# Kernel tuning notes

Hardware: AMD Instinct MI355X
Metric: run time of the kernel (lower is better)

Reference implementation:

```python
import jax, jax.numpy as jnp
import numpy as np

H = 256  # rnn_size


def setup_inputs() -> dict:
    key = jax.random.key(0)
    ks = jax.random.split(key, 6)
    B, T, F, D = 64, 512, 64, 64
    s_in = 1.0 / np.sqrt(F)
    s_rec = 1.0 / np.sqrt(H)
    return {
        "x": jax.random.normal(ks[0], (B, T, F), jnp.float32),
        "kernel": jax.random.normal(ks[1], (F, 3 * H), jnp.float32) * s_in,
        "recurrent_kernel": jax.random.normal(ks[2], (H, 3 * H), jnp.float32) * s_rec,
        "bias": jax.random.normal(ks[3], (3 * H,), jnp.float32) * 0.01,
        "dense_w": jax.random.normal(ks[4], (H, D), jnp.float32) * s_rec,
        "dense_b": jax.random.normal(ks[5], (D,), jnp.float32) * 0.01,
    }


def _gru_scan(x, kernel, recurrent_kernel, bias):
    B, T, _ = x.shape
    # Pre-project all timesteps: [B, T, 3H]
    xproj = jnp.einsum("btf,fg->btg", x, kernel) + bias
    xproj_t = jnp.transpose(xproj, (1, 0, 2))  # [T, B, 3H]

    def step(h, xt):
        # Keras GRU, reset_after=False: r gates the recurrent matmul of the candidate
        rec = h @ recurrent_kernel  # [B, 3H]
        xz, xr, xh = xt[:, :H], xt[:, H:2 * H], xt[:, 2 * H:]
        rz, rr, rh = rec[:, :H], rec[:, H:2 * H], rec[:, 2 * H:]
        z = jax.nn.sigmoid(xz + rz)
        r = jax.nn.sigmoid(xr + rr)
        hh = jnp.tanh(xh + r * rh)
        h_new = z * h + (1.0 - z) * hh
        return h_new, h_new

    h0 = jnp.zeros((B, H), x.dtype)
    h_last, outs = jax.lax.scan(step, h0, xproj_t)
    return jnp.transpose(outs, (1, 0, 2)), h_last  # [B,T,H], [B,H]


def reference(x, kernel, recurrent_kernel, bias, dense_w, dense_b):
    outputs, h_last = _gru_scan(x, kernel, recurrent_kernel, bias)
    state = jnp.tanh(h_last @ dense_w + dense_b)  # [B, dense_size]
    return outputs, state
```

## Files before the change

### kernel.cpp

```cpp
#include <hip/hip_runtime.h>


typedef _Float16 half2_t __attribute__((ext_vector_type(2)));
typedef _Float16 f16x4_t __attribute__((ext_vector_type(4)));

#define LOG2E 1.4426950408889634f

__device__ __forceinline__ float fast_sigmoid(float x) {
  float e = __builtin_amdgcn_exp2f(-x * LOG2E);
  return __builtin_amdgcn_rcpf(1.0f + e);
}
__device__ __forceinline__ float fast_tanh(float x) {
  float e = __builtin_amdgcn_exp2f(x * (2.0f * LOG2E));
  return 1.0f - 2.0f * __builtin_amdgcn_rcpf(1.0f + e);
}

__global__ __launch_bounds__(256, 4) void xproj_gemm(
    const float* __restrict__ x, const float* __restrict__ kmat,
    const float* __restrict__ bias, _Float16* __restrict__ xp) {
  __shared__ half2_t As2[32][132];
  __shared__ half2_t Bs2[32][132];
  const int tid = threadIdx.x;
  const int rb = blockIdx.x * 128;
  const int cb = blockIdx.y * 128;

  {
    const int k4 = (tid & 15) * 4;
    const int r0 = tid >> 4;
#pragma unroll
    for (int p = 0; p < 8; ++p) {
      int r = r0 + p * 16;
      float4 v = *(const float4*)(x + (size_t)(rb + r) * 64 + k4);
      half2_t lo, hi;
      lo[0] = (_Float16)v.x; lo[1] = (_Float16)v.y;
      hi[0] = (_Float16)v.z; hi[1] = (_Float16)v.w;
      As2[k4 / 2][r] = lo;
      As2[k4 / 2 + 1][r] = hi;
    }
  }
  {
    const int c4 = (tid & 31) * 4;
    const int kp0 = tid >> 5;
#pragma unroll
    for (int p = 0; p < 4; ++p) {
      int kp = kp0 + p * 8;
      float4 va = *(const float4*)(kmat + (size_t)(2 * kp) * 768 + cb + c4);
      float4 vb = *(const float4*)(kmat + (size_t)(2 * kp + 1) * 768 + cb + c4);
      half2_t o0, o1, o2, o3;
      o0[0] = (_Float16)va.x; o0[1] = (_Float16)vb.x;
      o1[0] = (_Float16)va.y; o1[1] = (_Float16)vb.y;
      o2[0] = (_Float16)va.z; o2[1] = (_Float16)vb.z;
      o3[0] = (_Float16)va.w; o3[1] = (_Float16)vb.w;
      Bs2[kp][c4 + 0] = o0;
      Bs2[kp][c4 + 1] = o1;
      Bs2[kp][c4 + 2] = o2;
      Bs2[kp][c4 + 3] = o3;
    }
  }
  __syncthreads();

  const int tx = tid & 15, ty = tid >> 4;
  const int r0 = ty * 8;
  const int c0 = tx * 4;
  float acc[8][8];
  {
    float4 b0 = *(const float4*)(bias + cb + c0);
    float4 b1 = *(const float4*)(bias + cb + 64 + c0);
    float bz[8] = {b0.x, b0.y, b0.z, b0.w, b1.x, b1.y, b1.z, b1.w};
#pragma unroll
    for (int i = 0; i < 8; ++i)
#pragma unroll
      for (int j = 0; j < 8; ++j) acc[i][j] = bz[j];
  }

#pragma unroll 2
  for (int kp = 0; kp < 32; ++kp) {
    half2_t a2[8], b2[8];
    *(int4*)(&a2[0]) = *(const int4*)(&As2[kp][r0]);
    *(int4*)(&a2[4]) = *(const int4*)(&As2[kp][r0 + 4]);
    *(int2*)(&b2[0]) = *(const int2*)(&Bs2[kp][c0]);
    *(int2*)(&b2[2]) = *(const int2*)(&Bs2[kp][c0 + 2]);
    *(int2*)(&b2[4]) = *(const int2*)(&Bs2[kp][64 + c0]);
    *(int2*)(&b2[6]) = *(const int2*)(&Bs2[kp][64 + c0 + 2]);
#pragma unroll
    for (int i = 0; i < 8; ++i)
#pragma unroll
      for (int j = 0; j < 8; ++j)
        acc[i][j] = __builtin_amdgcn_fdot2(a2[i], b2[j], acc[i][j], false);
  }

#pragma unroll
  for (int i = 0; i < 8; ++i) {
    f16x4_t o0, o1;
#pragma unroll
    for (int j = 0; j < 4; ++j) {
      o0[j] = (_Float16)acc[i][j];
      o1[j] = (_Float16)acc[i][4 + j];
    }
    _Float16* dst = xp + (size_t)(rb + r0 + i) * 768 + cb;
    *(f16x4_t*)(dst + c0) = o0;
    *(f16x4_t*)(dst + 64 + c0) = o1;
  }
}

__global__ __launch_bounds__(1024, 4) void gru_scan(
    const _Float16* __restrict__ xp, const float* __restrict__ wr,
    const float* __restrict__ dw, const float* __restrict__ db,
    float* __restrict__ out, float* __restrict__ state) {
  __shared__ float part[4 * 768];
  __shared__ float hbuf[256];
  __shared__ alignas(16) _Float16 hhalf[256];
  __shared__ _Float16 xrow[768];

  const int tid = threadIdx.x;
  const int b = blockIdx.x;
  const int c = tid >> 8;
  const int col = tid & 255;

  half2_t w2[3][32];
#pragma unroll
  for (int q = 0; q < 3; ++q) {
    const float* wp = wr + (size_t)(c * 64) * 768 + col + q * 256;
#pragma unroll
    for (int j = 0; j < 32; ++j) {
      float wa = wp[(size_t)(2 * j) * 768];
      float wb = wp[(size_t)(2 * j + 1) * 768];
      half2_t p;
      p[0] = (_Float16)wa;
      p[1] = (_Float16)wb;
      w2[q][j] = p;
    }
  }

  if (tid < 256) hhalf[tid] = (_Float16)0.0f;
  __syncthreads();

  const _Float16* xpb = xp + (size_t)b * 512 * 768;
  float* outb = out + (size_t)b * 512 * 256;
  const int4* hp2 = (const int4*)hhalf + c * 8;
  float hprev = 0.0f;

  for (int t = 0; t < 512; ++t) {
    _Float16 xv = (_Float16)0.0f;
    if (tid < 768) xv = xpb[(size_t)t * 768 + tid];

    float a0 = 0.0f, a1 = 0.0f, a2 = 0.0f;
    int4 hv = hp2[0];
#pragma unroll
    for (int g = 0; g < 8; ++g) {
      __builtin_amdgcn_sched_barrier(1);
      int4 hn = hv;
      if (g < 7) hn = hp2[g + 1];
      half2_t p0 = __builtin_bit_cast(half2_t, hv.x);
      half2_t p1 = __builtin_bit_cast(half2_t, hv.y);
      half2_t p2 = __builtin_bit_cast(half2_t, hv.z);
      half2_t p3 = __builtin_bit_cast(half2_t, hv.w);
      a0 = __builtin_amdgcn_fdot2(p0, w2[0][g * 4 + 0], a0, false);
      a0 = __builtin_amdgcn_fdot2(p1, w2[0][g * 4 + 1], a0, false);
      a0 = __builtin_amdgcn_fdot2(p2, w2[0][g * 4 + 2], a0, false);
      a0 = __builtin_amdgcn_fdot2(p3, w2[0][g * 4 + 3], a0, false);
      a1 = __builtin_amdgcn_fdot2(p0, w2[1][g * 4 + 0], a1, false);
      a1 = __builtin_amdgcn_fdot2(p1, w2[1][g * 4 + 1], a1, false);
      a1 = __builtin_amdgcn_fdot2(p2, w2[1][g * 4 + 2], a1, false);
      a1 = __builtin_amdgcn_fdot2(p3, w2[1][g * 4 + 3], a1, false);
      a2 = __builtin_amdgcn_fdot2(p0, w2[2][g * 4 + 0], a2, false);
      a2 = __builtin_amdgcn_fdot2(p1, w2[2][g * 4 + 1], a2, false);
      a2 = __builtin_amdgcn_fdot2(p2, w2[2][g * 4 + 2], a2, false);
      a2 = __builtin_amdgcn_fdot2(p3, w2[2][g * 4 + 3], a2, false);
      hv = hn;
    }
    part[c * 768 + col] = a0;
    part[c * 768 + col + 256] = a1;
    part[c * 768 + col + 512] = a2;
    if (tid < 768) xrow[tid] = xv;
    __syncthreads();

    if (tid < 256) {
      const int i = tid;
      if (t) outb[(size_t)(t - 1) * 256 + i] = hprev;
      float rz = part[i] + part[768 + i] + part[1536 + i] + part[2304 + i];
      float rr = part[256 + i] + part[768 + 256 + i] + part[1536 + 256 + i] +
                 part[2304 + 256 + i];
      float rh = part[512 + i] + part[768 + 512 + i] + part[1536 + 512 + i] +
                 part[2304 + 512 + i];
      float xz = (float)xrow[i];
      float xr = (float)xrow[256 + i];
      float xh = (float)xrow[512 + i];
      float z = fast_sigmoid(xz + rz);
      float r = fast_sigmoid(xr + rr);
      float hh = fast_tanh(xh + r * rh);
      float hnew = z * hprev + (1.0f - z) * hh;
      hprev = hnew;
      hhalf[i] = (_Float16)hnew;
    }
    __syncthreads();
  }

  if (tid < 256) {
    outb[(size_t)511 * 256 + tid] = hprev;
    hbuf[tid] = hprev;
  }
  __syncthreads();

  if (tid < 64) {
    float acc = db[tid];
#pragma unroll 8
    for (int k = 0; k < 256; ++k) acc = fmaf(hbuf[k], dw[k * 64 + tid], acc);
    state[(size_t)b * 64 + tid] = fast_tanh(acc);
  }
}

extern "C" void kernel_launch(void* const* d_in, const int* in_sizes, int n_in,
                              void* d_out, int out_size, void* d_ws,
                              size_t ws_size, hipStream_t stream) {
  const float* x = (const float*)d_in[0];
  const float* kmat = (const float*)d_in[1];
  const float* wr = (const float*)d_in[2];
  const float* bias = (const float*)d_in[3];
  const float* dw = (const float*)d_in[4];
  const float* db = (const float*)d_in[5];

  float* out = (float*)d_out;
  float* state = out + (size_t)64 * 512 * 256;
  _Float16* xp = (_Float16*)d_ws;

  dim3 gg(32768 / 128, 768 / 128);
  xproj_gemm<<<gg, 256, 0, stream>>>(x, kmat, bias, xp);
  gru_scan<<<64, 1024, 0, stream>>>(xp, wr, dw, db, out, state);
}
```

Measured before the change: 662.3 us.

## Reduce GRU recurrent partials with DPP in registers and double-buffer hidden state

Reorganizes the scan kernel so each lane covers a 32-element K-slice for six gate columns. The K-split partial sums are now reduced across lanes with DPP shuffles instead of through a shared-memory partial buffer. The hidden state is double-buffered in padded shared memory, which cuts each timestep from two barriers to one and drops the xrow staging. The trade-offs are more per-lane accumulators and select logic, and only a quarter of the lanes doing the gate math.

Result: slower. 964.9 us (+45.7%).

```diff
diff --git a/kernel.cpp b/kernel.cpp
--- a/kernel.cpp
+++ b/kernel.cpp
@@ -13,6 +13,13 @@
 __device__ __forceinline__ float fast_tanh(float x) {
   float e = __builtin_amdgcn_exp2f(x * (2.0f * LOG2E));
   return 1.0f - 2.0f * __builtin_amdgcn_rcpf(1.0f + e);
+}
+
+template <int CTRL>
+__device__ __forceinline__ float dpp_xor_add(float v) {
+  int s = __builtin_amdgcn_update_dpp(0, __builtin_bit_cast(int, v), CTRL,
+                                      0xF, 0xF, false);
+  return v + __builtin_bit_cast(float, s);
 }
 
 __global__ __launch_bounds__(256, 4) void xproj_gemm(
@@ -103,102 +110,143 @@
   }
 }
 
+#define DOT4(U, J)                                                \
+  do {                                                            \
+    half2_t p0 = __builtin_bit_cast(half2_t, (U).x);              \
+    half2_t p1 = __builtin_bit_cast(half2_t, (U).y);              \
+    half2_t p2 = __builtin_bit_cast(half2_t, (U).z);              \
+    half2_t p3 = __builtin_bit_cast(half2_t, (U).w);               \
+    a0 = __builtin_amdgcn_fdot2(p0, w2[0][(J) + 0], a0, false);   \
+    a0 = __builtin_amdgcn_fdot2(p1, w2[0][(J) + 1], a0, false);   \
+    a0 = __builtin_amdgcn_fdot2(p2, w2[0][(J) + 2], a0, false);   \
+    a0 = __builtin_amdgcn_fdot2(p3, w2[0][(J) + 3], a0, false);   \
+    a1 = __builtin_amdgcn_fdot2(p0, w2[1][(J) + 0], a1, false);   \
+    a1 = __builtin_amdgcn_fdot2(p1, w2[1][(J) + 1], a1, false);   \
+    a1 = __builtin_amdgcn_fdot2(p2, w2[1][(J) + 2], a1, false);   \
+    a1 = __builtin_amdgcn_fdot2(p3, w2[1][(J) + 3], a1, false);   \
+    a2 = __builtin_amdgcn_fdot2(p0, w2[2][(J) + 0], a2, false);   \
+    a2 = __builtin_amdgcn_fdot2(p1, w2[2][(J) + 1], a2, false);   \
+    a2 = __builtin_amdgcn_fdot2(p2, w2[2][(J) + 2], a2, false);   \
+    a2 = __builtin_amdgcn_fdot2(p3, w2[2][(J) + 3], a2, false);   \
+    a3 = __builtin_amdgcn_fdot2(p0, w2[3][(J) + 0], a3, false);   \
+    a3 = __builtin_amdgcn_fdot2(p1, w2[3][(J) + 1], a3, false);   \
+    a3 = __builtin_amdgcn_fdot2(p2, w2[3][(J) + 2], a3, false);   \
+    a3 = __builtin_amdgcn_fdot2(p3, w2[3][(J) + 3], a3, false);   \
+    a4 = __builtin_amdgcn_fdot2(p0, w2[4][(J) + 0], a4, false);   \
+    a4 = __builtin_amdgcn_fdot2(p1, w2[4][(J) + 1], a4, false);   \
+    a4 = __builtin_amdgcn_fdot2(p2, w2[4][(J) + 2], a4, false);   \
+    a4 = __builtin_amdgcn_fdot2(p3, w2[4][(J) + 3], a4, false);   \
+    a5 = __builtin_amdgcn_fdot2(p0, w2[5][(J) + 0], a5, false);   \
+    a5 = __builtin_amdgcn_fdot2(p1, w2[5][(J) + 1], a5, false);   \
+    a5 = __builtin_amdgcn_fdot2(p2, w2[5][(J) + 2], a5, false);   \
+    a5 = __builtin_amdgcn_fdot2(p3, w2[5][(J) + 3], a5, false);   \
+  } while (0)
+
 __global__ __launch_bounds__(1024, 4) void gru_scan(
     const _Float16* __restrict__ xp, const float* __restrict__ wr,
     const float* __restrict__ dw, const float* __restrict__ db,
     float* __restrict__ out, float* __restrict__ state) {
-  __shared__ float part[4 * 768];
+  __shared__ alignas(16) _Float16 hh[2][8][40];
   __shared__ float hbuf[256];
-  __shared__ alignas(16) _Float16 hhalf[256];
-  __shared__ _Float16 xrow[768];
 
   const int tid = threadIdx.x;
   const int b = blockIdx.x;
-  const int c = tid >> 8;
-  const int col = tid & 255;
-
-  half2_t w2[3][32];
-#pragma unroll
-  for (int q = 0; q < 3; ++q) {
-    const float* wp = wr + (size_t)(c * 64) * 768 + col + q * 256;
-#pragma unroll
-    for (int j = 0; j < 32; ++j) {
-      float wa = wp[(size_t)(2 * j) * 768];
-      float wb = wp[(size_t)(2 * j + 1) * 768];
+  const int lane = tid & 63;
+  const int wave = tid >> 6;
+  const int c = (lane & 3) | ((lane >> 1) & 4);
+  const int sidx = ((lane >> 2) & 1) | ((lane >> 3) & 6);
+  const int cidx = wave * 8 + sidx;
+  const int hb = (lane >> 3) & 1;
+  const bool gl = ((lane & 3) == 0);
+  const int col = cidx + hb * 128;
+
+  half2_t w2[6][16];
+#pragma unroll
+  for (int q = 0; q < 6; ++q) {
+    const int g = q % 3, hbq = q / 3;
+    const float* wp = wr + (size_t)(c * 32) * 768 + g * 256 + cidx + hbq * 128;
+#pragma unroll
+    for (int j = 0; j < 16; ++j) {
       half2_t p;
-      p[0] = (_Float16)wa;
-      p[1] = (_Float16)wb;
+      p[0] = (_Float16)wp[(size_t)(2 * j) * 768];
+      p[1] = (_Float16)wp[(size_t)(2 * j + 1) * 768];
       w2[q][j] = p;
     }
   }
 
-  if (tid < 256) hhalf[tid] = (_Float16)0.0f;
+  if (tid < 640) ((_Float16*)hh)[tid] = (_Float16)0.0f;
   __syncthreads();
 
-  const _Float16* xpb = xp + (size_t)b * 512 * 768;
-  float* outb = out + (size_t)b * 512 * 256;
-  const int4* hp2 = (const int4*)hhalf + c * 8;
+  const _Float16* xp_b = xp + (size_t)b * 512 * 768;
+  float* out_b = out + (size_t)b * 512 * 256;
+
   float hprev = 0.0f;
-
+  int buf = 0;
+
+#pragma unroll 1
   for (int t = 0; t < 512; ++t) {
-    _Float16 xv = (_Float16)0.0f;
-    if (tid < 768) xv = xpb[(size_t)t * 768 + tid];
-
-    float a0 = 0.0f, a1 = 0.0f, a2 = 0.0f;
-    int4 hv = hp2[0];
-#pragma unroll
-    for (int g = 0; g < 8; ++g) {
-      __builtin_amdgcn_sched_barrier(1);
-      int4 hn = hv;
-      if (g < 7) hn = hp2[g + 1];
-      half2_t p0 = __builtin_bit_cast(half2_t, hv.x);
-      half2_t p1 = __builtin_bit_cast(half2_t, hv.y);
-      half2_t p2 = __builtin_bit_cast(half2_t, hv.z);
-      half2_t p3 = __builtin_bit_cast(half2_t, hv.w);
-      a0 = __builtin_amdgcn_fdot2(p0, w2[0][g * 4 + 0], a0, false);
-      a0 = __builtin_amdgcn_fdot2(p1, w2[0][g * 4 + 1], a0, false);
-      a0 = __builtin_amdgcn_fdot2(p2, w2[0][g * 4 + 2], a0, false);
-      a0 = __builtin_amdgcn_fdot2(p3, w2[0][g * 4 + 3], a0, false);
-      a1 = __builtin_amdgcn_fdot2(p0, w2[1][g * 4 + 0], a1, false);
-      a1 = __builtin_amdgcn_fdot2(p1, w2[1][g * 4 + 1], a1, false);
-      a1 = __builtin_amdgcn_fdot2(p2, w2[1][g * 4 + 2], a1, false);
-      a1 = __builtin_amdgcn_fdot2(p3, w2[1][g * 4 + 3], a1, false);
-      a2 = __builtin_amdgcn_fdot2(p0, w2[2][g * 4 + 0], a2, false);
-      a2 = __builtin_amdgcn_fdot2(p1, w2[2][g * 4 + 1], a2, false);
-      a2 = __builtin_amdgcn_fdot2(p2, w2[2][g * 4 + 2], a2, false);
-      a2 = __builtin_amdgcn_fdot2(p3, w2[2][g * 4 + 3], a2, false);
-      hv = hn;
-    }
-    part[c * 768 + col] = a0;
-    part[c * 768 + col + 256] = a1;
-    part[c * 768 + col + 512] = a2;
-    if (tid < 768) xrow[tid] = xv;
+    _Float16 x0h = (_Float16)0.0f, x1h = (_Float16)0.0f, x2h = (_Float16)0.0f;
+    if (gl) {
+      if (t) out_b[(size_t)(t - 1) * 256 + col] = hprev;
+      const _Float16* xr_ = xp_b + (size_t)t * 768 + col;
+      x0h = xr_[0];
+      x1h = xr_[256];
+      x2h = xr_[512];
+    }
+
+    const int4* hp = (const int4*)hh[buf][c];
+    float a0 = 0.f, a1 = 0.f, a2 = 0.f, a3 = 0.f, a4 = 0.f, a5 = 0.f;
+    {
+      int4 u0 = hp[0];
+      int4 u1 = hp[1];
+      DOT4(u0, 0);
+      DOT4(u1, 4);
+    }
+    __builtin_amdgcn_sched_barrier(0);
+    {
+      int4 u2 = hp[2];
+      int4 u3 = hp[3];
+      DOT4(u2, 8);
+      DOT4(u3, 12);
+    }
+
+    a0 = dpp_xor_add<0xB1>(a0);
+    a1 = dpp_xor_add<0xB1>(a1);
+    a2 = dpp_xor_add<0xB1>(a2);
+    a3 = dpp_xor_add<0xB1>(a3);
+    a4 = dpp_xor_add<0xB1>(a4);
+    a5 = dpp_xor_add<0xB1>(a5);
+    a0 = dpp_xor_add<0x4E>(a0);
+    a1 = dpp_xor_add<0x4E>(a1);
+    a2 = dpp_xor_add<0x4E>(a2);
+    a3 = dpp_xor_add<0x4E>(a3);
+    a4 = dpp_xor_add<0x4E>(a4);
+    a5 = dpp_xor_add<0x4E>(a5);
+    a0 = dpp_xor_add<0x128>(a0);
+    a1 = dpp_xor_add<0x128>(a1);
+    a2 = dpp_xor_add<0x128>(a2);
+    a3 = dpp_xor_add<0x128>(a3);
+    a4 = dpp_xor_add<0x128>(a4);
+    a5 = dpp_xor_add<0x128>(a5);
+
+    if (gl) {
+      float rz = hb ? a3 : a0;
+      float rr = hb ? a4 : a1;
+      float rh = hb ? a5 : a2;
+      float z = fast_sigmoid((float)x0h + rz);
+      float r = fast_sigmoid((float)x1h + rr);
+      float hcand = fast_tanh((float)x2h + r * rh);
+      float hnew = z * hprev + (1.0f - z) * hcand;
+      hprev = hnew;
+      hh[buf ^ 1][col >> 5][col & 31] = (_Float16)hnew;
+    }
     __syncthreads();
-
-    if (tid < 256) {
-      const int i = tid;
-      if (t) outb[(size_t)(t - 1) * 256 + i] = hprev;
-      float rz = part[i] + part[768 + i] + part[1536 + i] + part[2304 + i];
-      float rr = part[256 + i] + part[768 + 256 + i] + part[1536 + 256 + i] +
-                 part[2304 + 256 + i];
-      float rh = part[512 + i] + part[768 + 512 + i] + part[1536 + 512 + i] +
-                 part[2304 + 512 + i];
-      float xz = (float)xrow[i];
-      float xr = (float)xrow[256 + i];
-      float xh = (float)xrow[512 + i];
-      float z = fast_sigmoid(xz + rz);
-      float r = fast_sigmoid(xr + rr);
-      float hh = fast_tanh(xh + r * rh);
-      float hnew = z * hprev + (1.0f - z) * hh;
-      hprev = hnew;
-      hhalf[i] = (_Float16)hnew;
-    }
-    __syncthreads();
-  }
-
-  if (tid < 256) {
-    outb[(size_t)511 * 256 + tid] = hprev;
-    hbuf[tid] = hprev;
+    buf ^= 1;
+  }
+
+  if (gl) {
+    out_b[(size_t)511 * 256 + col] = hprev;
+    hbuf[col] = hprev;
   }
   __syncthreads();
 
```

## Compute GRU recurrent matvec with MFMA and double-buffered hidden state

Applied to the files above, without the earlier changes.

The recurrent h@W step now runs on 16x16x32 f16 MFMA instructions. Each of 16 waves owns 16 output columns and keeps its weight slice in registers. The A operand's only nonzero row holds h, so most of each MFMA's work is padding. Double-buffering the hidden state removes one of the two block barriers per timestep, and the cross-wave partial-sum reduction through shared memory goes away. In exchange, only 16 lanes per wave run the gate math and load x, and most of the MFMA throughput is spent on zeros.

Result: slower. 733.9 us (+10.8%).

```diff
diff --git a/kernel.cpp b/kernel.cpp
--- a/kernel.cpp
+++ b/kernel.cpp
@@ -3,6 +3,8 @@
 
 typedef _Float16 half2_t __attribute__((ext_vector_type(2)));
 typedef _Float16 f16x4_t __attribute__((ext_vector_type(4)));
+typedef _Float16 f16x8_t __attribute__((ext_vector_type(8)));
+typedef float f32x4_t __attribute__((ext_vector_type(4)));
 
 #define LOG2E 1.4426950408889634f
 
@@ -107,98 +109,84 @@
     const _Float16* __restrict__ xp, const float* __restrict__ wr,
     const float* __restrict__ dw, const float* __restrict__ db,
     float* __restrict__ out, float* __restrict__ state) {
-  __shared__ float part[4 * 768];
+  __shared__ alignas(16) _Float16 zz[256];
+  __shared__ alignas(16) _Float16 hh0[256];
+  __shared__ alignas(16) _Float16 hh1[256];
   __shared__ float hbuf[256];
-  __shared__ alignas(16) _Float16 hhalf[256];
-  __shared__ _Float16 xrow[768];
 
   const int tid = threadIdx.x;
   const int b = blockIdx.x;
-  const int c = tid >> 8;
-  const int col = tid & 255;
-
-  half2_t w2[3][32];
-#pragma unroll
-  for (int q = 0; q < 3; ++q) {
-    const float* wp = wr + (size_t)(c * 64) * 768 + col + q * 256;
-#pragma unroll
-    for (int j = 0; j < 32; ++j) {
-      float wa = wp[(size_t)(2 * j) * 768];
-      float wb = wp[(size_t)(2 * j + 1) * 768];
-      half2_t p;
-      p[0] = (_Float16)wa;
-      p[1] = (_Float16)wb;
-      w2[q][j] = p;
-    }
-  }
-
-  if (tid < 256) hhalf[tid] = (_Float16)0.0f;
+  const int lane = tid & 63;
+  const int w = tid >> 6;
+  const int q = lane >> 4;
+  const int col = w * 16 + (lane & 15);
+  const bool gl = (lane < 16);
+
+  f16x8_t wf[3][8];
+#pragma unroll
+  for (int g = 0; g < 3; ++g)
+#pragma unroll
+    for (int s = 0; s < 8; ++s) {
+      const float* wp = wr + (size_t)(s * 32 + q * 8) * 768 + g * 256 + col;
+      f16x8_t v;
+#pragma unroll
+      for (int j = 0; j < 8; ++j) v[j] = (_Float16)wp[(size_t)j * 768];
+      wf[g][s] = v;
+    }
+
+  if (tid < 256) {
+    zz[tid] = (_Float16)0.0f;
+    hh0[tid] = (_Float16)0.0f;
+  }
   __syncthreads();
+
+  const bool arow0 = ((lane & 15) == 0);
+  const _Float16* ab0 = (arow0 ? hh0 : zz) + q * 8;
+  const _Float16* ab1 = (arow0 ? hh1 : zz) + q * 8;
 
   const _Float16* xpb = xp + (size_t)b * 512 * 768;
   float* outb = out + (size_t)b * 512 * 256;
-  const int4* hp2 = (const int4*)hhalf + c * 8;
   float hprev = 0.0f;
 
+#pragma unroll 2
   for (int t = 0; t < 512; ++t) {
-    _Float16 xv = (_Float16)0.0f;
-    if (tid < 768) xv = xpb[(size_t)t * 768 + tid];
-
-    float a0 = 0.0f, a1 = 0.0f, a2 = 0.0f;
-    int4 hv = hp2[0];
-#pragma unroll
-    for (int g = 0; g < 8; ++g) {
-      __builtin_amdgcn_sched_barrier(1);
-      int4 hn = hv;
-      if (g < 7) hn = hp2[g + 1];
-      half2_t p0 = __builtin_bit_cast(half2_t, hv.x);
-      half2_t p1 = __builtin_bit_cast(half2_t, hv.y);
-      half2_t p2 = __builtin_bit_cast(half2_t, hv.z);
-      half2_t p3 = __builtin_bit_cast(half2_t, hv.w);
-      a0 = __builtin_amdgcn_fdot2(p0, w2[0][g * 4 + 0], a0, false);
-      a0 = __builtin_amdgcn_fdot2(p1, w2[0][g * 4 + 1], a0, false);
-      a0 = __builtin_amdgcn_fdot2(p2, w2[0][g * 4 + 2], a0, false);
-      a0 = __builtin_amdgcn_fdot2(p3, w2[0][g * 4 + 3], a0, false);
-      a1 = __builtin_amdgcn_fdot2(p0, w2[1][g * 4 + 0], a1, false);
-      a1 = __builtin_amdgcn_fdot2(p1, w2[1][g * 4 + 1], a1, false);
-      a1 = __builtin_amdgcn_fdot2(p2, w2[1][g * 4 + 2], a1, false);
-      a1 = __builtin_amdgcn_fdot2(p3, w2[1][g * 4 + 3], a1, false);
-      a2 = __builtin_amdgcn_fdot2(p0, w2[2][g * 4 + 0], a2, false);
-      a2 = __builtin_amdgcn_fdot2(p1, w2[2][g * 4 + 1], a2, false);
-      a2 = __builtin_amdgcn_fdot2(p2, w2[2][g * 4 + 2], a2, false);
-      a2 = __builtin_amdgcn_fdot2(p3, w2[2][g * 4 + 3], a2, false);
-      hv = hn;
-    }
-    part[c * 768 + col] = a0;
-    part[c * 768 + col + 256] = a1;
-    part[c * 768 + col + 512] = a2;
-    if (tid < 768) xrow[tid] = xv;
+    const _Float16* ab = (t & 1) ? ab1 : ab0;
+    _Float16* hw = (t & 1) ? hh0 : hh1;
+
+    _Float16 xz = (_Float16)0.0f, xr = (_Float16)0.0f, xh = (_Float16)0.0f;
+    if (gl) {
+      if (t) outb[(size_t)(t - 1) * 256 + col] = hprev;
+      const _Float16* xq = xpb + (size_t)t * 768 + col;
+      xz = xq[0];
+      xr = xq[256];
+      xh = xq[512];
+    }
+
+    f32x4_t az = {0.f, 0.f, 0.f, 0.f};
+    f32x4_t ar = {0.f, 0.f, 0.f, 0.f};
+    f32x4_t ah = {0.f, 0.f, 0.f, 0.f};
+#pragma unroll
+    for (int s = 0; s < 8; ++s) {
+      f16x8_t a = *(const f16x8_t*)(ab + s * 32);
+      az = __builtin_amdgcn_mfma_f32_16x16x32_f16(a, wf[0][s], az, 0, 0, 0);
+      ar = __builtin_amdgcn_mfma_f32_16x16x32_f16(a, wf[1][s], ar, 0, 0, 0);
+      ah = __builtin_amdgcn_mfma_f32_16x16x32_f16(a, wf[2][s], ah, 0, 0, 0);
+    }
+
+    if (gl) {
+      float z = fast_sigmoid((float)xz + az[0]);
+      float r = fast_sigmoid((float)xr + ar[0]);
+      float hcand = fast_tanh((float)xh + r * ah[0]);
+      float hnew = z * hprev + (1.0f - z) * hcand;
+      hprev = hnew;
+      hw[col] = (_Float16)hnew;
+    }
     __syncthreads();
-
-    if (tid < 256) {
-      const int i = tid;
-      if (t) outb[(size_t)(t - 1) * 256 + i] = hprev;
-      float rz = part[i] + part[768 + i] + part[1536 + i] + part[2304 + i];
-      float rr = part[256 + i] + part[768 + 256 + i] + part[1536 + 256 + i] +
-                 part[2304 + 256 + i];
-      float rh = part[512 + i] + part[768 + 512 + i] + part[1536 + 512 + i] +
-                 part[2304 + 512 + i];
-      float xz = (float)xrow[i];
-      float xr = (float)xrow[256 + i];
-      float xh = (float)xrow[512 + i];
-      float z = fast_sigmoid(xz + rz);
-      float r = fast_sigmoid(xr + rr);
-      float hh = fast_tanh(xh + r * rh);
-      float hnew = z * hprev + (1.0f - z) * hh;
-      hprev = hnew;
-      hhalf[i] = (_Float16)hnew;
-    }
-    __syncthreads();
-  }
-
-  if (tid < 256) {
-    outb[(size_t)511 * 256 + tid] = hprev;
-    hbuf[tid] = hprev;
+  }
+
+  if (gl) {
+    outb[(size_t)511 * 256 + col] = hprev;
+    hbuf[col] = hprev;
   }
   __syncthreads();
 
```
